# Performance work log

Hardware: AMD Instinct MI355X
Metric: run time of the kernel (lower is better)

Reference implementation:

```python
import jax, jax.numpy as jnp
import numpy as np

D_MODEL = 1024
N_HEAD = 16
B, T = 4, 1024
MAX_REL = 32  # max_relative_positions


def setup_inputs() -> dict:
    key = jax.random.key(0)
    ks = jax.random.split(key, 12)
    s = 0.02
    inp = {
        "x": jax.random.normal(ks[0], (B, T, D_MODEL), jnp.float32),
        "mask": jnp.tril(jnp.ones((T, T), dtype=bool)),  # causal mask, 1 = keep
        "Wq": jax.random.normal(ks[1], (D_MODEL, D_MODEL), jnp.float32) * s,
        "bq": jax.random.normal(ks[2], (D_MODEL,), jnp.float32) * s,
        "Wk": jax.random.normal(ks[3], (D_MODEL, D_MODEL), jnp.float32) * s,
        "bk": jax.random.normal(ks[4], (D_MODEL,), jnp.float32) * s,
        "Wv": jax.random.normal(ks[5], (D_MODEL, D_MODEL), jnp.float32) * s,
        "bv": jax.random.normal(ks[6], (D_MODEL,), jnp.float32) * s,
        "Wo": jax.random.normal(ks[7], (D_MODEL, D_MODEL), jnp.float32) * s,
        "bo": jax.random.normal(ks[8], (D_MODEL,), jnp.float32) * s,
        "rel_bias": jax.random.normal(ks[9], (2 * MAX_REL - 1, N_HEAD), jnp.float32) * s,
        "n_head": N_HEAD,
    }
    return inp


def reference(x, mask, Wq, bq, Wk, bk, Wv, bv, Wo, bo, rel_bias, n_head):
    Bx, Tx, C = x.shape
    Dh = C // n_head
    scale = Dh ** (-0.5)
    # projections: torch Linear is x @ W.T + b
    Q = (x @ Wq.T + bq).reshape(Bx, Tx, n_head, Dh)
    K = (x @ Wk.T + bk).reshape(Bx, Tx, n_head, Dh)
    V = (x @ Wv.T + bv).reshape(Bx, Tx, n_head, Dh)
    # scores: [B, H, T, T]
    scores = jnp.einsum("bqhd,bkhd->bhqk", Q, K) * scale
    # T5-style clipped relative-position bias
    pos = jnp.arange(Tx)
    rel = pos[None, :] - pos[:, None]                     # k_pos - q_pos, [T, T]
    buckets = jnp.clip(rel, -(MAX_REL - 1), MAX_REL - 1) + (MAX_REL - 1)
    bias = rel_bias[buckets]                              # [T, T, H]
    scores = scores + jnp.transpose(bias, (2, 0, 1))[None]
    # original applies masked_fill(-inf) then masked_fill(0): net effect = 0
    scores = jnp.where(mask, scores, 0.0)
    w = jax.nn.relu(scores) + 1e-6
    w = jnp.where(mask, w, 0.0)
    w = w / (jnp.sum(w, axis=-1, keepdims=True) + 1e-6)
    out = jnp.einsum("bhqk,bkhd->bqhd", w, V).reshape(Bx, Tx, C)
    return out @ Wo.T + bo
```

## Files before the change

### kernel.cpp

```cpp
#include <hip/hip_runtime.h>


typedef __attribute__((ext_vector_type(8))) __bf16 bf16x8;
typedef __attribute__((ext_vector_type(4))) __bf16 bf16x4;
typedef __attribute__((ext_vector_type(4))) float f32x4;
typedef unsigned short u16;

__device__ __forceinline__ u16 f2bf(float f) {
  unsigned u = __float_as_uint(f);
  u += 0x7FFFu + ((u >> 16) & 1u);
  return (u16)(u >> 16);
}
__device__ __forceinline__ float bf2f(u16 b) {
  return __uint_as_float(((unsigned)b) << 16);
}
__device__ __forceinline__ void gl_lds16(const void* g, void* l) {
  __builtin_amdgcn_global_load_lds((__attribute__((address_space(1))) void*)g,
                                   (__attribute__((address_space(3))) void*)l,
                                   16, 0, 0);
}

__global__ __launch_bounds__(256) void cast_all_kernel(
    const float* __restrict__ x,  const float* __restrict__ wq,
    const float* __restrict__ wk, const float* __restrict__ wv,
    const float* __restrict__ wo,
    u16* __restrict__ xb, u16* __restrict__ wqb, u16* __restrict__ wkb,
    u16* __restrict__ wvb, u16* __restrict__ wob) {
  long i4 = (long)blockIdx.x * 256 + threadIdx.x;
  const float* src; u16* dst; long rel;
  if (i4 < 1048576) { src = x; dst = xb; rel = i4; }
  else {
    long j = i4 - 1048576;
    int w = (int)(j >> 18);
    rel = j & 262143;
    src = (w == 0) ? wq : (w == 1) ? wk : (w == 2) ? wv : wo;
    dst = (w == 0) ? wqb : (w == 1) ? wkb : (w == 2) ? wvb : wob;
  }
  float4 v = ((const float4*)src)[rel];
  ushort4 o;
  o.x = f2bf(v.x); o.y = f2bf(v.y); o.z = f2bf(v.z); o.w = f2bf(v.w);
  ((ushort4*)dst)[rel] = o;
}

template <bool STORE_BF16>
__global__ __launch_bounds__(256) void gemm_fast(
    const u16* __restrict__ A,
    const u16* __restrict__ B0, const u16* __restrict__ B1, const u16* __restrict__ B2,
    const float* __restrict__ b0, const float* __restrict__ b1,
    const float* __restrict__ b2,
    void* __restrict__ C0, void* __restrict__ C1, void* __restrict__ C2) {
  constexpr int K = 1024;
  __shared__ __align__(16) u16 As[128 * 64];
  __shared__ __align__(16) u16 Bs[128 * 64];

  const int m0 = blockIdx.x * 128;
  const int sel = blockIdx.y >> 3;
  const int nloc = (blockIdx.y & 7) * 128;
  const u16* B = sel == 0 ? B0 : sel == 1 ? B1 : B2;
  const float* bias = sel == 0 ? b0 : sel == 1 ? b1 : b2;
  void* Cout = sel == 0 ? C0 : sel == 1 ? C1 : C2;

  const int t = threadIdx.x;
  const int lane = t & 63;
  const int wv = t >> 6;
  const int quad = lane >> 4;
  const int l15 = lane & 15;
  const int wr = wv >> 1, wc = wv & 1;

  const f32x4 vzero = {0.f, 0.f, 0.f, 0.f};
  f32x4 acc[4][4];
#pragma unroll
  for (int i = 0; i < 4; ++i)
#pragma unroll
    for (int j = 0; j < 4; ++j) acc[i][j] = vzero;

  for (int kt = 0; kt < K / 64; ++kt) {
    const int k0 = kt * 64;
#pragma unroll
    for (int p = 0; p < 4; ++p) {
      int idx = t + p * 256;
      int row = idx >> 3, seg = idx & 7;
      gl_lds16(&A[(long)(m0 + row) * K + k0 + seg * 8], &As[idx * 8]);
      gl_lds16(&B[(long)(nloc + row) * K + k0 + seg * 8], &Bs[idx * 8]);
    }
    __syncthreads();
#pragma unroll
    for (int ks = 0; ks < 64; ks += 32) {
      bf16x8 af[4], bfg[4];
#pragma unroll
      for (int i = 0; i < 4; ++i)
        af[i] = *(const bf16x8*)&As[(wr * 64 + i * 16 + l15) * 64 + ks + quad * 8];
#pragma unroll
      for (int j = 0; j < 4; ++j)
        bfg[j] = *(const bf16x8*)&Bs[(wc * 64 + j * 16 + l15) * 64 + ks + quad * 8];
#pragma unroll
      for (int i = 0; i < 4; ++i)
#pragma unroll
        for (int j = 0; j < 4; ++j)
          acc[i][j] = __builtin_amdgcn_mfma_f32_16x16x32_bf16(af[i], bfg[j], acc[i][j], 0, 0, 0);
    }
    __syncthreads();
  }

  float bv[4];
#pragma unroll
  for (int j = 0; j < 4; ++j) bv[j] = bias[nloc + wc * 64 + j * 16 + l15];

#pragma unroll
  for (int i = 0; i < 4; ++i) {
#pragma unroll
    for (int r = 0; r < 4; ++r) {
      int row = m0 + wr * 64 + i * 16 + quad * 4 + r;
      long base = (long)row * 1024 + nloc + wc * 64;
#pragma unroll
      for (int j = 0; j < 4; ++j) {
        float v = acc[i][j][r] + bv[j];
        if (STORE_BF16) ((u16*)Cout)[base + j * 16 + l15] = f2bf(v);
        else            ((float*)Cout)[base + j * 16 + l15] = v;
      }
    }
  }
}

__global__ __launch_bounds__(256) void attn_split(
    const u16* __restrict__ Qb,
    const u16* __restrict__ Kb,
    const u16* __restrict__ Vb,
    const float* __restrict__ rel_bias,
    u16* __restrict__ att,
    u16* __restrict__ Opart,
    float* __restrict__ Dpart) {
  constexpr int VS = 68;
  __shared__ __align__(16) u16 Ks[64 * 64];
  __shared__ __align__(16) u16 Vt[64 * VS];
  __shared__ __align__(16) u16 Ws[4][16 * 64];
  __shared__ float biasl[64];

  const int bx = blockIdx.x;
  const int bh = bx / 24;
  const int slot = bx - bh * 24;
  const int b = bh >> 4, h = bh & 15;

  int qb, cbeg, cend, pidx;
  bool multi;
  if (slot < 8) { qb = slot; cbeg = 0; cend = qb; multi = false; pidx = 0; }
  else {
    int s = slot - 8;
    qb = 8 + (s >> 1);
    int part = s & 1;
    multi = true;
    pidx = (bh * 8 + (qb - 8)) * 2 + part;
    if (part == 0) { cbeg = 0; cend = 7; }
    else           { cbeg = 8; cend = qb; }
  }
  const int q0 = qb * 64;

  const int t = threadIdx.x;
  const int lane = t & 63;
  const int wv = t >> 6;
  const int quad = lane >> 4;
  const int l15 = lane & 15;

  if (t < 63) biasl[t] = rel_bias[t * 16 + h];

  const long qrow = (long)(b * 1024 + q0 + wv * 16 + l15) * 1024 + h * 64;
  bf16x8 qf0 = *(const bf16x8*)&Qb[qrow + quad * 8];
  bf16x8 qf1 = *(const bf16x8*)&Qb[qrow + 32 + quad * 8];

  const f32x4 vzero = {0.f, 0.f, 0.f, 0.f};
  f32x4 acc_o[4];
#pragma unroll
  for (int j = 0; j < 4; ++j) acc_o[j] = vzero;
  f32x4 denom = vzero;
  const float scale = 0.125f;
  const int myq = q0 + wv * 16 + quad * 4;

  for (int c = cbeg; c <= cend; ++c) {
    const int k0 = c * 64;
    if (c != cbeg) __syncthreads();
#pragma unroll
    for (int p = 0; p < 2; ++p) {
      int idx = t + p * 256;
      int row = idx >> 3, seg = idx & 7;
      gl_lds16(&Kb[(long)(b * 1024 + k0 + row) * 1024 + h * 64 + seg * 8], &Ks[idx * 8]);
    }
#pragma unroll
    for (int p = 0; p < 2; ++p) {
      int seg = lane >> 3;
      int krel = (lane & 7) + (p * 4 + wv) * 8;
      uint4 vvld = *(const uint4*)&Vb[(long)(b * 1024 + k0 + krel) * 1024 + h * 64 + seg * 8];
      const u16* u = (const u16*)&vvld;
#pragma unroll
      for (int j = 0; j < 8; ++j) Vt[(seg * 8 + j) * VS + krel] = u[j];
    }
    __syncthreads();

#pragma unroll
    for (int g = 0; g < 4; ++g) {
      bf16x8 kf0 = *(const bf16x8*)&Ks[(g * 16 + l15) * 64 + quad * 8];
      bf16x8 kf1 = *(const bf16x8*)&Ks[(g * 16 + l15) * 64 + 32 + quad * 8];
      f32x4 s = vzero;
      s = __builtin_amdgcn_mfma_f32_16x16x32_bf16(qf0, kf0, s, 0, 0, 0);
      s = __builtin_amdgcn_mfma_f32_16x16x32_bf16(qf1, kf1, s, 0, 0, 0);
      const int kg = k0 + g * 16 + l15;
#pragma unroll
      for (int r = 0; r < 4; ++r) {
        int q = myq + r;
        int dd = kg - q;
        dd = dd < -31 ? -31 : (dd > 31 ? 31 : dd);
        float sv = s[r] * scale + biasl[dd + 31];
        float w = (kg <= q) ? (fmaxf(sv, 0.f) + 1e-6f) : 0.f;
        u16 wb = f2bf(w);
        denom[r] += bf2f(wb);
        Ws[wv][(quad * 4 + r) * 64 + g * 16 + l15] = wb;
      }
    }
    asm volatile("s_waitcnt lgkmcnt(0)" ::: "memory");
#pragma unroll
    for (int ks = 0; ks < 64; ks += 32) {
      bf16x8 aw = *(const bf16x8*)&Ws[wv][l15 * 64 + ks + quad * 8];
#pragma unroll
      for (int j = 0; j < 4; ++j) {
        union { bf16x8 v8; bf16x4 v4[2]; } bu;
        int vbase = (j * 16 + l15) * VS + ks + quad * 8;
        bu.v4[0] = *(const bf16x4*)&Vt[vbase];
        bu.v4[1] = *(const bf16x4*)&Vt[vbase + 4];
        acc_o[j] = __builtin_amdgcn_mfma_f32_16x16x32_bf16(aw, bu.v8, acc_o[j], 0, 0, 0);
      }
    }
  }

#pragma unroll
  for (int m = 1; m < 16; m <<= 1)
#pragma unroll
    for (int r = 0; r < 4; ++r) denom[r] += __shfl_xor(denom[r], m);

  if (!multi) {
    float inv[4];
#pragma unroll
    for (int r = 0; r < 4; ++r) inv[r] = 1.f / (denom[r] + 1e-6f);
#pragma unroll
    for (int j = 0; j < 4; ++j)
#pragma unroll
      for (int r = 0; r < 4; ++r) {
        int q = myq + r;
        att[(long)(b * 1024 + q) * 1024 + h * 64 + j * 16 + l15] = f2bf(acc_o[j][r] * inv[r]);
      }
  } else {
    const int qrel = wv * 16 + quad * 4;
#pragma unroll
    for (int j = 0; j < 4; ++j)
#pragma unroll
      for (int r = 0; r < 4; ++r)
        Opart[(long)pidx * 4096 + (qrel + r) * 64 + j * 16 + l15] = f2bf(acc_o[j][r]);
    if (l15 == 0) {
#pragma unroll
      for (int r = 0; r < 4; ++r) Dpart[pidx * 64 + qrel + r] = denom[r];
    }
  }
}

__global__ __launch_bounds__(256) void attn_reduce(
    const u16* __restrict__ Opart, const float* __restrict__ Dpart,
    u16* __restrict__ att) {
  const int bx = blockIdx.x;
  const int bh = bx >> 3;
  const int q8 = bx & 7;
  const int b = bh >> 4, h = bh & 15;
  const int qb = 8 + q8;
  const int pidx = (bh * 8 + q8) * 2;

  const int t = threadIdx.x;
  const int row = t >> 2;
  const int dseg = t & 3;

  const float d0 = Dpart[pidx * 64 + row];
  const float d1 = Dpart[(pidx + 1) * 64 + row];
  const float inv = 1.f / (d0 + d1 + 1e-6f);

  const u16* O0 = Opart + (long)pidx * 4096 + row * 64 + dseg * 16;
  const u16* O1 = O0 + 4096;
  union { uint4 q[2]; u16 s[16]; } a, c, o;
  a.q[0] = *(const uint4*)O0;       a.q[1] = *(const uint4*)(O0 + 8);
  c.q[0] = *(const uint4*)O1;       c.q[1] = *(const uint4*)(O1 + 8);
#pragma unroll
  for (int i = 0; i < 16; ++i) o.s[i] = f2bf((bf2f(a.s[i]) + bf2f(c.s[i])) * inv);
  u16* dst = att + (long)(b * 1024 + qb * 64 + row) * 1024 + h * 64 + dseg * 16;
  *(uint4*)dst = o.q[0];
  *(uint4*)(dst + 8) = o.q[1];
}

extern "C" void kernel_launch(void* const* d_in, const int* in_sizes, int n_in,
                              void* d_out, int out_size, void* d_ws, size_t ws_size,
                              hipStream_t stream) {
  const float* x  = (const float*)d_in[0];
  const float* Wq = (const float*)d_in[2];
  const float* bq = (const float*)d_in[3];
  const float* Wk = (const float*)d_in[4];
  const float* bk = (const float*)d_in[5];
  const float* Wv = (const float*)d_in[6];
  const float* bv = (const float*)d_in[7];
  const float* Wo = (const float*)d_in[8];
  const float* bo = (const float*)d_in[9];
  const float* rb = (const float*)d_in[10];

  char* ws = (char*)d_ws;
  u16* xb    = (u16*)(ws);
  u16* Opart = (u16*)(ws);
  u16* wqb   = (u16*)(ws + (8l  << 20));
  float* Dpart = (float*)(ws + (8l << 20));
  u16* wkb   = (u16*)(ws + (10l << 20));
  u16* wvb   = (u16*)(ws + (12l << 20));
  u16* wob   = (u16*)(ws + (14l << 20));
  u16* Qb    = (u16*)(ws + (16l << 20));
  u16* Kb    = (u16*)d_out;
  u16* Vb    = (u16*)((char*)d_out + (8l << 20));

  cast_all_kernel<<<8192, 256, 0, stream>>>(x, Wq, Wk, Wv, Wo, xb, wqb, wkb, wvb, wob);
  gemm_fast<true><<<dim3(32, 24), 256, 0, stream>>>(
      xb, wqb, wkb, wvb, bq, bk, bv, Qb, Kb, Vb);
  attn_split<<<1536, 256, 0, stream>>>(Qb, Kb, Vb, rb, Qb, Opart, Dpart);
  attn_reduce<<<512, 256, 0, stream>>>(Opart, Dpart, Qb);
  gemm_fast<false><<<dim3(32, 8), 256, 0, stream>>>(
      Qb, wob, wob, wob, bo, bo, bo, d_out, d_out, d_out);
}
```

Baseline: 225.8 us.

## Produce V pre-transposed in QKV GEMM and load it via async LDS copies

The QKV projection now computes V as Wv·xᵀ, so V lands in global memory already transposed (head-dim major, ldc 4096) with a per-row bias. The attention kernel can then stream V tiles straight into LDS with global_load_lds instead of loading through registers and scattering them transposed with scalar 16-bit LDS stores. The padded stride moves from the V tile to the per-wave weight tile. The cost is a strided store pattern for the V output in the GEMM epilogue and splitting the templated GEMM into two specialised kernels.

Result: no change. 229.6 us (+1.7%).

```diff
diff --git a/kernel.cpp b/kernel.cpp
--- a/kernel.cpp
+++ b/kernel.cpp
@@ -42,23 +42,33 @@
   ((ushort4*)dst)[rel] = o;
 }
 
-template <bool STORE_BF16>
-__global__ __launch_bounds__(256) void gemm_fast(
-    const u16* __restrict__ A,
-    const u16* __restrict__ B0, const u16* __restrict__ B1, const u16* __restrict__ B2,
-    const float* __restrict__ b0, const float* __restrict__ b1,
-    const float* __restrict__ b2,
-    void* __restrict__ C0, void* __restrict__ C1, void* __restrict__ C2) {
+__global__ __launch_bounds__(256) void gemm_qkv(
+    const u16* __restrict__ xb, const u16* __restrict__ wqb,
+    const u16* __restrict__ wkb, const u16* __restrict__ wvb,
+    const float* __restrict__ bq, const float* __restrict__ bk,
+    const float* __restrict__ bv,
+    u16* __restrict__ Qb, u16* __restrict__ Kb, u16* __restrict__ Vtg) {
   constexpr int K = 1024;
   __shared__ __align__(16) u16 As[128 * 64];
   __shared__ __align__(16) u16 Bs[128 * 64];
 
-  const int m0 = blockIdx.x * 128;
-  const int sel = blockIdx.y >> 3;
-  const int nloc = (blockIdx.y & 7) * 128;
-  const u16* B = sel == 0 ? B0 : sel == 1 ? B1 : B2;
-  const float* bias = sel == 0 ? b0 : sel == 1 ? b1 : b2;
-  void* Cout = sel == 0 ? C0 : sel == 1 ? C1 : C2;
+  const int bx = blockIdx.x;
+  const u16 *AT, *BT;
+  const float* bias;
+  u16* C;
+  int m0, n0, ldc;
+  bool rowbias;
+  if (bx < 512) {
+    int sel = bx >> 8, rem = bx & 255;
+    m0 = (rem >> 3) * 128; n0 = (rem & 7) * 128;
+    AT = xb; BT = sel ? wkb : wqb; bias = sel ? bk : bq;
+    C = sel ? Kb : Qb; ldc = 1024; rowbias = false;
+  } else {
+    int rem = bx - 512;
+    m0 = (rem >> 5) * 128; n0 = (rem & 31) * 128;
+    AT = wvb; BT = xb; bias = bv;
+    C = Vtg; ldc = 4096; rowbias = true;
+  }
 
   const int t = threadIdx.x;
   const int lane = t & 63;
@@ -80,8 +90,8 @@
     for (int p = 0; p < 4; ++p) {
       int idx = t + p * 256;
       int row = idx >> 3, seg = idx & 7;
-      gl_lds16(&A[(long)(m0 + row) * K + k0 + seg * 8], &As[idx * 8]);
-      gl_lds16(&B[(long)(nloc + row) * K + k0 + seg * 8], &Bs[idx * 8]);
+      gl_lds16(&AT[(long)(m0 + row) * K + k0 + seg * 8], &As[idx * 8]);
+      gl_lds16(&BT[(long)(n0 + row) * K + k0 + seg * 8], &Bs[idx * 8]);
     }
     __syncthreads();
 #pragma unroll
@@ -102,22 +112,93 @@
     __syncthreads();
   }
 
-  float bv[4];
-#pragma unroll
-  for (int j = 0; j < 4; ++j) bv[j] = bias[nloc + wc * 64 + j * 16 + l15];
+  float cb[4];
+  if (!rowbias) {
+#pragma unroll
+    for (int j = 0; j < 4; ++j) cb[j] = bias[n0 + wc * 64 + j * 16 + l15];
+  }
 
 #pragma unroll
   for (int i = 0; i < 4; ++i) {
 #pragma unroll
     for (int r = 0; r < 4; ++r) {
       int row = m0 + wr * 64 + i * 16 + quad * 4 + r;
-      long base = (long)row * 1024 + nloc + wc * 64;
+      long base = (long)row * ldc + n0 + wc * 64;
+      float rb_ = rowbias ? bias[row] : 0.f;
 #pragma unroll
       for (int j = 0; j < 4; ++j) {
-        float v = acc[i][j][r] + bv[j];
-        if (STORE_BF16) ((u16*)Cout)[base + j * 16 + l15] = f2bf(v);
-        else            ((float*)Cout)[base + j * 16 + l15] = v;
+        float v = acc[i][j][r] + (rowbias ? rb_ : cb[j]);
+        C[base + j * 16 + l15] = f2bf(v);
       }
+    }
+  }
+}
+
+__global__ __launch_bounds__(256) void gemm_out(
+    const u16* __restrict__ A, const u16* __restrict__ B,
+    const float* __restrict__ bias, float* __restrict__ C) {
+  constexpr int K = 1024;
+  __shared__ __align__(16) u16 As[128 * 64];
+  __shared__ __align__(16) u16 Bs[128 * 64];
+
+  const int m0 = blockIdx.x * 128;
+  const int n0 = blockIdx.y * 128;
+
+  const int t = threadIdx.x;
+  const int lane = t & 63;
+  const int wv = t >> 6;
+  const int quad = lane >> 4;
+  const int l15 = lane & 15;
+  const int wr = wv >> 1, wc = wv & 1;
+
+  const f32x4 vzero = {0.f, 0.f, 0.f, 0.f};
+  f32x4 acc[4][4];
+#pragma unroll
+  for (int i = 0; i < 4; ++i)
+#pragma unroll
+    for (int j = 0; j < 4; ++j) acc[i][j] = vzero;
+
+  for (int kt = 0; kt < K / 64; ++kt) {
+    const int k0 = kt * 64;
+#pragma unroll
+    for (int p = 0; p < 4; ++p) {
+      int idx = t + p * 256;
+      int row = idx >> 3, seg = idx & 7;
+      gl_lds16(&A[(long)(m0 + row) * K + k0 + seg * 8], &As[idx * 8]);
+      gl_lds16(&B[(long)(n0 + row) * K + k0 + seg * 8], &Bs[idx * 8]);
+    }
+    __syncthreads();
+#pragma unroll
+    for (int ks = 0; ks < 64; ks += 32) {
+      bf16x8 af[4], bfg[4];
+#pragma unroll
+      for (int i = 0; i < 4; ++i)
+        af[i] = *(const bf16x8*)&As[(wr * 64 + i * 16 + l15) * 64 + ks + quad * 8];
+#pragma unroll
+      for (int j = 0; j < 4; ++j)
+        bfg[j] = *(const bf16x8*)&Bs[(wc * 64 + j * 16 + l15) * 64 + ks + quad * 8];
+#pragma unroll
+      for (int i = 0; i < 4; ++i)
+#pragma unroll
+        for (int j = 0; j < 4; ++j)
+          acc[i][j] = __builtin_amdgcn_mfma_f32_16x16x32_bf16(af[i], bfg[j], acc[i][j], 0, 0, 0);
+    }
+    __syncthreads();
+  }
+
+  float cb[4];
+#pragma unroll
+  for (int j = 0; j < 4; ++j) cb[j] = bias[n0 + wc * 64 + j * 16 + l15];
+
+#pragma unroll
+  for (int i = 0; i < 4; ++i) {
+#pragma unroll
+    for (int r = 0; r < 4; ++r) {
+      int row = m0 + wr * 64 + i * 16 + quad * 4 + r;
+      long base = (long)row * 1024 + n0 + wc * 64;
+#pragma unroll
+      for (int j = 0; j < 4; ++j)
+        C[base + j * 16 + l15] = acc[i][j][r] + cb[j];
     }
   }
 }
@@ -125,15 +206,15 @@
 __global__ __launch_bounds__(256) void attn_split(
     const u16* __restrict__ Qb,
     const u16* __restrict__ Kb,
-    const u16* __restrict__ Vb,
+    const u16* __restrict__ Vtg,
     const float* __restrict__ rel_bias,
     u16* __restrict__ att,
     u16* __restrict__ Opart,
     float* __restrict__ Dpart) {
-  constexpr int VS = 68;
+  constexpr int WS = 68;
   __shared__ __align__(16) u16 Ks[64 * 64];
-  __shared__ __align__(16) u16 Vt[64 * VS];
-  __shared__ __align__(16) u16 Ws[4][16 * 64];
+  __shared__ __align__(16) u16 Vts[64 * 64];
+  __shared__ __align__(16) u16 Ws[4][16 * WS];
   __shared__ float biasl[64];
 
   const int bx = blockIdx.x;
@@ -186,12 +267,9 @@
     }
 #pragma unroll
     for (int p = 0; p < 2; ++p) {
-      int seg = lane >> 3;
-      int krel = (lane & 7) + (p * 4 + wv) * 8;
-      uint4 vvld = *(const uint4*)&Vb[(long)(b * 1024 + k0 + krel) * 1024 + h * 64 + seg * 8];
-      const u16* u = (const u16*)&vvld;
-#pragma unroll
-      for (int j = 0; j < 8; ++j) Vt[(seg * 8 + j) * VS + krel] = u[j];
+      int idx = t + p * 256;
+      int row = idx >> 3, seg = idx & 7;
+      gl_lds16(&Vtg[(long)(h * 64 + row) * 4096 + b * 1024 + k0 + seg * 8], &Vts[idx * 8]);
     }
     __syncthreads();
 
@@ -212,20 +290,20 @@
         float w = (kg <= q) ? (fmaxf(sv, 0.f) + 1e-6f) : 0.f;
         u16 wb = f2bf(w);
         denom[r] += bf2f(wb);
-        Ws[wv][(quad * 4 + r) * 64 + g * 16 + l15] = wb;
+        Ws[wv][(quad * 4 + r) * WS + g * 16 + l15] = wb;
       }
     }
     asm volatile("s_waitcnt lgkmcnt(0)" ::: "memory");
 #pragma unroll
     for (int ks = 0; ks < 64; ks += 32) {
-      bf16x8 aw = *(const bf16x8*)&Ws[wv][l15 * 64 + ks + quad * 8];
+      union { bf16x8 v8; bf16x4 v4[2]; } au;
+      int wbase = l15 * WS + ks + quad * 8;
+      au.v4[0] = *(const bf16x4*)&Ws[wv][wbase];
+      au.v4[1] = *(const bf16x4*)&Ws[wv][wbase + 4];
 #pragma unroll
       for (int j = 0; j < 4; ++j) {
-        union { bf16x8 v8; bf16x4 v4[2]; } bu;
-        int vbase = (j * 16 + l15) * VS + ks + quad * 8;
-        bu.v4[0] = *(const bf16x4*)&Vt[vbase];
-        bu.v4[1] = *(const bf16x4*)&Vt[vbase + 4];
-        acc_o[j] = __builtin_amdgcn_mfma_f32_16x16x32_bf16(aw, bu.v8, acc_o[j], 0, 0, 0);
+        bf16x8 bvv = *(const bf16x8*)&Vts[(j * 16 + l15) * 64 + ks + quad * 8];
+        acc_o[j] = __builtin_amdgcn_mfma_f32_16x16x32_bf16(au.v8, bvv, acc_o[j], 0, 0, 0);
       }
     }
   }
@@ -305,22 +383,20 @@
   const float* rb = (const float*)d_in[10];
 
   char* ws = (char*)d_ws;
-  u16* xb    = (u16*)(ws);
-  u16* Opart = (u16*)(ws);
-  u16* wqb   = (u16*)(ws + (8l  << 20));
+  u16* xb      = (u16*)(ws);
+  u16* Opart   = (u16*)(ws);
+  u16* wqb     = (u16*)(ws + (8l  << 20));
   float* Dpart = (float*)(ws + (8l << 20));
-  u16* wkb   = (u16*)(ws + (10l << 20));
-  u16* wvb   = (u16*)(ws + (12l << 20));
-  u16* wob   = (u16*)(ws + (14l << 20));
-  u16* Qb    = (u16*)(ws + (16l << 20));
-  u16* Kb    = (u16*)d_out;
-  u16* Vb    = (u16*)((char*)d_out + (8l << 20));
+  u16* wkb     = (u16*)(ws + (10l << 20));
+  u16* wvb     = (u16*)(ws + (12l << 20));
+  u16* wob     = (u16*)(ws + (14l << 20));
+  u16* Qb      = (u16*)(ws + (16l << 20));
+  u16* Kb      = (u16*)d_out;
+  u16* Vtg     = (u16*)((char*)d_out + (8l << 20));
 
   cast_all_kernel<<<8192, 256, 0, stream>>>(x, Wq, Wk, Wv, Wo, xb, wqb, wkb, wvb, wob);
-  gemm_fast<true><<<dim3(32, 24), 256, 0, stream>>>(
-      xb, wqb, wkb, wvb, bq, bk, bv, Qb, Kb, Vb);
-  attn_split<<<1536, 256, 0, stream>>>(Qb, Kb, Vb, rb, Qb, Opart, Dpart);
+  gemm_qkv<<<768, 256, 0, stream>>>(xb, wqb, wkb, wvb, bq, bk, bv, Qb, Kb, Vtg);
+  attn_split<<<1536, 256, 0, stream>>>(Qb, Kb, Vtg, rb, Qb, Opart, Dpart);
   attn_reduce<<<512, 256, 0, stream>>>(Opart, Dpart, Qb);
-  gemm_fast<false><<<dim3(32, 8), 256, 0, stream>>>(
-      Qb, wob, wob, wob, bo, bo, bo, d_out, d_out, d_out);
-}
+  gemm_out<<<dim3(32, 8), 256, 0, stream>>>(Qb, wob, bo, (float*)d_out);
+}
```
